# Kernel tuning notes

Hardware: AMD Instinct MI355X
Metric: run time of the kernel (lower is better)

## Reference

```python
import jax, jax.numpy as jnp
import numpy as np

N_PARTICLES = 256
N_DIM = 3
N_KERNELS = 256   # hidden_dim
N_TOUT = 20       # number of time RBF kernels (n_out)
CUTOFF = 5.0
GAMMA = 0.3
BATCH = 4

# off-diagonal column indices: idx[i, j] = j + (j >= i), shape [N, N-1]
_cols = np.arange(N_PARTICLES - 1)
OFFDIAG_IDX = _cols[None, :] + (_cols[None, :] >= np.arange(N_PARTICLES)[:, None])


def setup_inputs() -> dict:
    key = jax.random.key(0)
    k1, k2, k3 = jax.random.split(key, 3)
    x = jax.random.normal(k1, (BATCH, N_PARTICLES * N_DIM), dtype=jnp.float32)
    t = jax.random.uniform(k2, (BATCH,), dtype=jnp.float32)
    weights = jax.random.normal(k3, (N_KERNELS, N_TOUT), dtype=jnp.float32) * np.sqrt(1.0 / N_KERNELS)
    bias = jnp.zeros((1, N_TOUT), dtype=jnp.float32)
    importance = jnp.zeros((N_KERNELS,), dtype=jnp.float32)
    mus = jnp.linspace(0.0, CUTOFF, N_KERNELS, dtype=jnp.float32)
    neg_log_gammas = -jnp.log(GAMMA * jnp.ones((N_KERNELS,), dtype=jnp.float32))
    mus_time = jnp.linspace(0.0, 1.0, N_TOUT, dtype=jnp.float32)
    neg_log_gammas_time = -jnp.log(GAMMA * jnp.ones((N_TOUT,), dtype=jnp.float32))
    return dict(x=x, t=t, weights=weights, bias=bias, importance=importance,
                mus=mus, neg_log_gammas=neg_log_gammas,
                mus_time=mus_time, neg_log_gammas_time=neg_log_gammas_time)


def _rbf_kernels(d, mu, neg_log_gamma):
    # d: [..., 1], mu/neg_log_gamma: [K] -> normalized kernels [..., K]
    inv_gamma2 = jnp.exp(neg_log_gamma) ** 2
    rbfs = jnp.exp(-(d - mu) ** 2 * inv_gamma2)
    return rbfs / (1e-6 + rbfs.sum(axis=-1, keepdims=True))


def reference(x, t, weights, bias, importance, mus, neg_log_gammas,
              mus_time, neg_log_gammas_time):
    B = x.shape[0]
    xp = x.reshape(B, N_PARTICLES, N_DIM)
    # all-pairs distance vectors x_i - x_j, then drop the diagonal -> [B, N, N-1, D]
    r_full = xp[:, :, None, :] - xp[:, None, :, :]
    r = r_full[:, jnp.arange(N_PARTICLES)[:, None], OFFDIAG_IDX, :]
    # distances [B, N, N-1, 1]
    d = jnp.sqrt((r ** 2).sum(axis=-1) + 1e-6)[..., None]
    # normalized distance RBFs [B, N, N-1, K]
    kernels = _rbf_kernels(d, mus, neg_log_gammas)
    # force magnitude over time-output channels [B, N, N-1, T]
    force_mag = (kernels + importance ** 2) @ weights + bias
    # time RBFs [B, T] -> weight and reduce over T
    trbfs = _rbf_kernels(t[:, None], mus_time, neg_log_gammas_time)
    force_mag = (force_mag * trbfs[:, None, None, :]).sum(axis=-1, keepdims=True)
    # weighted aggregation over neighbor axis -> forces [B, N, D]
    forces = (r * force_mag).sum(axis=-2)
    return forces
```

## Files before the change

### kernel.cpp

```cpp
#include <hip/hip_runtime.h>
#include <hip/hip_bf16.h>
#include <stdint.h>

#define NP     256
#define NK     256
#define NT     20
#define BATCHN 4
#define LOG2E  1.44269504088896340736f

typedef __hip_bfloat16 bf16;
typedef float v2f __attribute__((ext_vector_type(2)));

__device__ __forceinline__ bool probe_f32(const void* mus) {
    return ((const uint32_t*)mus)[0] == 0u;
}

__device__ __forceinline__ float ldf(const void* p, int idx, bool f32) {
    return f32 ? ((const float*)p)[idx]
               : __bfloat162float(((const bf16*)p)[idx]);
}

__global__ __launch_bounds__(256)
void vf_fused(const void* __restrict__ x,     const void* __restrict__ t_in,
              const void* __restrict__ weights, const void* __restrict__ bias,
              const void* __restrict__ importance, const void* __restrict__ mus,
              const void* __restrict__ nlg,   const void* __restrict__ mus_t,
              const void* __restrict__ nlg_t, void* __restrict__ out)
{
    const int tid = threadIdx.x;
    const int b   = blockIdx.x >> 8;
    const int i   = blockIdx.x & 255;
    const bool f32 = probe_f32(mus);

    __shared__ __align__(16) float s_pos[NP * 3];
    __shared__ __align__(16) float s_mu[NK];
    __shared__ __align__(16) float s_wp[NK];
    __shared__ float s_traw[NT];
    __shared__ float s_trbf[NT];
    __shared__ float s_redc[4];
    __shared__ float s_redf[12];
    __shared__ float s_constv;

    for (int idx = tid; idx < NP * 3; idx += 256)
        s_pos[idx] = ldf(x, b * NP * 3 + idx, f32);

    if (tid < NT) {
        float tv = ldf(t_in, b, f32);
        float mt = ldf(mus_t, tid, f32);
        float gt = __expf(ldf(nlg_t, tid, f32));
        float dd = tv - mt;
        s_traw[tid] = __expf(-dd * dd * gt * gt);
    }
    __syncthreads();
    if (tid < NT) {
        float s = 0.f;
        #pragma unroll
        for (int tt = 0; tt < NT; ++tt) s += s_traw[tt];
        s_trbf[tid] = s_traw[tid] / (1e-6f + s);
    }
    __syncthreads();

    {
        const int k = tid;
        float wp = 0.f;
        #pragma unroll
        for (int tt = 0; tt < NT; ++tt)
            wp = fmaf(ldf(weights, k * NT + tt, f32), s_trbf[tt], wp);

        s_mu[k] = ldf(mus, k, f32);
        s_wp[k] = wp;

        float imp = ldf(importance, k, f32);
        float v = imp * imp * wp;
        if (k < NT) v = fmaf(s_trbf[k], ldf(bias, k, f32), v);
        #pragma unroll
        for (int off = 32; off > 0; off >>= 1) v += __shfl_down(v, off);
        if ((k & 63) == 0) s_redc[k >> 6] = v;
    }
    __syncthreads();
    if (tid == 0) s_constv = s_redc[0] + s_redc[1] + s_redc[2] + s_redc[3];
    __syncthreads();

    const float g  = __expf(ldf(nlg, 0, f32));
    const float na = -(g * g) * LOG2E;

    float fx = 0.f, fy = 0.f, fz = 0.f;
    if (tid < NP - 1) {
        const int j = tid + (tid >= i ? 1 : 0);
        const float rx = s_pos[i * 3 + 0] - s_pos[j * 3 + 0];
        const float ry = s_pos[i * 3 + 1] - s_pos[j * 3 + 1];
        const float rz = s_pos[i * 3 + 2] - s_pos[j * 3 + 2];
        const float q  = rx * rx + ry * ry + rz * rz + 1e-6f;
        const float d  = sqrtf(q);

        const float4* mu4 = (const float4*)s_mu;
        const float4* wp4 = (const float4*)s_wp;
        const v2f d2v = {d, d};
        const v2f na2 = {na, na};
        v2f normA = {0.f, 0.f}, normB = {0.f, 0.f};
        v2f numA  = {0.f, 0.f}, numB  = {0.f, 0.f};

        #pragma unroll 4
        for (int p = 0; p < NK / 4; ++p) {
            const float4 m = mu4[p];
            const float4 w = wp4[p];
            const v2f muA = {m.x, m.y}, muB = {m.z, m.w};
            const v2f wpA = {w.x, w.y}, wpB = {w.z, w.w};
            const v2f dmA = d2v - muA, dmB = d2v - muB;
            const v2f agA = dmA * dmA * na2;
            const v2f agB = dmB * dmB * na2;
            const v2f eA = {exp2f(agA.x), exp2f(agA.y)};
            const v2f eB = {exp2f(agB.x), exp2f(agB.y)};
            normA += eA; normB += eB;
            numA  += eA * wpA;
            numB  += eB * wpB;
        }
        const float norm = normA.x + normA.y + normB.x + normB.y;
        const float num  = numA.x  + numA.y  + numB.x  + numB.y;
        const float fs = num / (1e-6f + norm) + s_constv;
        fx = rx * fs; fy = ry * fs; fz = rz * fs;
    }

    #pragma unroll
    for (int off = 32; off > 0; off >>= 1) {
        fx += __shfl_down(fx, off);
        fy += __shfl_down(fy, off);
        fz += __shfl_down(fz, off);
    }
    if ((tid & 63) == 0) {
        const int w = tid >> 6;
        s_redf[w * 3 + 0] = fx;
        s_redf[w * 3 + 1] = fy;
        s_redf[w * 3 + 2] = fz;
    }
    __syncthreads();
    if (tid < 3) {
        const float fv = s_redf[tid] + s_redf[3 + tid] + s_redf[6 + tid] + s_redf[9 + tid];
        const int o = (b * NP + i) * 3 + tid;
        if (f32) ((float*)out)[o] = fv;
        else     ((bf16*)out)[o]  = __float2bfloat16(fv);
    }
}

extern "C" void kernel_launch(void* const* d_in, const int* in_sizes, int n_in,
                              void* d_out, int out_size, void* d_ws, size_t ws_size,
                              hipStream_t stream)
{
    vf_fused<<<dim3(BATCHN * NP), dim3(256), 0, stream>>>(
        d_in[0], d_in[1], d_in[2], d_in[3], d_in[4],
        d_in[5], d_in[6], d_in[7], d_in[8], d_out);
}
```

Measured before the change: 93.13 us.

## Split per-batch time-weight precompute into separate prep kernel feeding force kernel

Moves the time-RBF weighting, the per-kernel weight projection and the constant term into a small prep kernel that runs once per batch and writes interleaved mu/wp pairs to workspace. The force kernel then reads those directly from global/L2 instead of recomputing them in every one of 1024 blocks, and drops the shared-memory staging and most syncthreads. It adds a second launch and relies on the workspace being large enough, with a fallback to the old fused kernel otherwise. Inner-loop operands now come from global memory instead of LDS, which may cost latency.

Result: no change. 94.42 us (+1.4%).

```diff
diff --git a/kernel.cpp b/kernel.cpp
--- a/kernel.cpp
+++ b/kernel.cpp
@@ -18,6 +18,132 @@
 __device__ __forceinline__ float ldf(const void* p, int idx, bool f32) {
     return f32 ? ((const float*)p)[idx]
                : __bfloat162float(((const bf16*)p)[idx]);
+}
+
+__global__ __launch_bounds__(256)
+void vf_prep(const void* __restrict__ t_in, const void* __restrict__ weights,
+             const void* __restrict__ bias, const void* __restrict__ importance,
+             const void* __restrict__ mus,  const void* __restrict__ mus_t,
+             const void* __restrict__ nlg_t, float* __restrict__ ws)
+{
+    const int tid = threadIdx.x;
+    const int b   = blockIdx.x;
+    const bool f32 = probe_f32(mus);
+
+    __shared__ float s_traw[NT];
+    __shared__ float s_trbf[NT];
+    __shared__ float s_redc[4];
+
+    if (tid < NT) {
+        float tv = ldf(t_in, b, f32);
+        float mt = ldf(mus_t, tid, f32);
+        float gt = __expf(ldf(nlg_t, tid, f32));
+        float dd = tv - mt;
+        s_traw[tid] = __expf(-dd * dd * gt * gt);
+    }
+    __syncthreads();
+    if (tid < NT) {
+        float s = 0.f;
+        #pragma unroll
+        for (int tt = 0; tt < NT; ++tt) s += s_traw[tt];
+        s_trbf[tid] = s_traw[tid] / (1e-6f + s);
+    }
+    __syncthreads();
+
+    const int k = tid;
+    float wp = 0.f;
+    #pragma unroll
+    for (int tt = 0; tt < NT; ++tt)
+        wp = fmaf(ldf(weights, k * NT + tt, f32), s_trbf[tt], wp);
+
+    float* cw = ws + b * (NK * 2);
+    cw[(k >> 2) * 8 + (k & 3)]     = ldf(mus, k, f32);
+    cw[(k >> 2) * 8 + 4 + (k & 3)] = wp;
+
+    float imp = ldf(importance, k, f32);
+    float v = imp * imp * wp;
+    if (k < NT) v = fmaf(s_trbf[k], ldf(bias, k, f32), v);
+    #pragma unroll
+    for (int off = 32; off > 0; off >>= 1) v += __shfl_down(v, off);
+    if ((k & 63) == 0) s_redc[k >> 6] = v;
+    __syncthreads();
+    if (tid == 0)
+        ws[BATCHN * NK * 2 + b] = s_redc[0] + s_redc[1] + s_redc[2] + s_redc[3];
+}
+
+__global__ __launch_bounds__(256)
+void vf_force(const void* __restrict__ x,  const void* __restrict__ mus,
+              const void* __restrict__ nlg, const float* __restrict__ ws,
+              void* __restrict__ out)
+{
+    const int tid = threadIdx.x;
+    const int b   = blockIdx.x >> 8;
+    const int i   = blockIdx.x & 255;
+    const bool f32 = probe_f32(mus);
+
+    __shared__ float s_redf[12];
+
+    const int xb = b * NP * 3;
+    const float pix = ldf(x, xb + i * 3 + 0, f32);
+    const float piy = ldf(x, xb + i * 3 + 1, f32);
+    const float piz = ldf(x, xb + i * 3 + 2, f32);
+
+    const int j = (tid < NP - 1) ? tid + (tid >= i ? 1 : 0) : i;
+    const float rx = pix - ldf(x, xb + j * 3 + 0, f32);
+    const float ry = piy - ldf(x, xb + j * 3 + 1, f32);
+    const float rz = piz - ldf(x, xb + j * 3 + 2, f32);
+    const float q  = rx * rx + ry * ry + rz * rz + 1e-6f;
+    const float d  = sqrtf(q);
+
+    const float g  = __expf(ldf(nlg, 0, f32));
+    const float na = -(g * g) * LOG2E;
+
+    const float4* cw4 = (const float4*)(ws + b * (NK * 2));
+    const v2f d2v = {d, d};
+    const v2f na2 = {na, na};
+    v2f normA = {0.f, 0.f}, normB = {0.f, 0.f};
+    v2f numA  = {0.f, 0.f}, numB  = {0.f, 0.f};
+
+    #pragma unroll 4
+    for (int p = 0; p < NK / 4; ++p) {
+        const float4 m = cw4[2 * p];
+        const float4 w = cw4[2 * p + 1];
+        const v2f muA = {m.x, m.y}, muB = {m.z, m.w};
+        const v2f wpA = {w.x, w.y}, wpB = {w.z, w.w};
+        const v2f dmA = d2v - muA, dmB = d2v - muB;
+        const v2f agA = dmA * dmA * na2;
+        const v2f agB = dmB * dmB * na2;
+        const v2f eA = {exp2f(agA.x), exp2f(agA.y)};
+        const v2f eB = {exp2f(agB.x), exp2f(agB.y)};
+        normA += eA; normB += eB;
+        numA  += eA * wpA;
+        numB  += eB * wpB;
+    }
+    const float norm = normA.x + normA.y + normB.x + normB.y;
+    const float num  = numA.x  + numA.y  + numB.x  + numB.y;
+    float fs = num / (1e-6f + norm) + ws[BATCHN * NK * 2 + b];
+    if (tid >= NP - 1) fs = 0.f;
+    float fx = rx * fs, fy = ry * fs, fz = rz * fs;
+
+    #pragma unroll
+    for (int off = 32; off > 0; off >>= 1) {
+        fx += __shfl_down(fx, off);
+        fy += __shfl_down(fy, off);
+        fz += __shfl_down(fz, off);
+    }
+    if ((tid & 63) == 0) {
+        const int w = tid >> 6;
+        s_redf[w * 3 + 0] = fx;
+        s_redf[w * 3 + 1] = fy;
+        s_redf[w * 3 + 2] = fz;
+    }
+    __syncthreads();
+    if (tid < 3) {
+        const float fv = s_redf[tid] + s_redf[3 + tid] + s_redf[6 + tid] + s_redf[9 + tid];
+        const int o = (b * NP + i) * 3 + tid;
+        if (f32) ((float*)out)[o] = fv;
+        else     ((bf16*)out)[o]  = __float2bfloat16(fv);
+    }
 }
 
 __global__ __launch_bounds__(256)
@@ -66,10 +192,8 @@
         #pragma unroll
         for (int tt = 0; tt < NT; ++tt)
             wp = fmaf(ldf(weights, k * NT + tt, f32), s_trbf[tt], wp);
-
         s_mu[k] = ldf(mus, k, f32);
         s_wp[k] = wp;
-
         float imp = ldf(importance, k, f32);
         float v = imp * imp * wp;
         if (k < NT) v = fmaf(s_trbf[k], ldf(bias, k, f32), v);
@@ -146,7 +270,16 @@
                               void* d_out, int out_size, void* d_ws, size_t ws_size,
                               hipStream_t stream)
 {
-    vf_fused<<<dim3(BATCHN * NP), dim3(256), 0, stream>>>(
-        d_in[0], d_in[1], d_in[2], d_in[3], d_in[4],
-        d_in[5], d_in[6], d_in[7], d_in[8], d_out);
-}
+    const size_t ws_need = (size_t)(BATCHN * NK * 2 + BATCHN) * sizeof(float);
+    if (d_ws != nullptr && ws_size >= ws_need) {
+        float* ws = (float*)d_ws;
+        vf_prep<<<dim3(BATCHN), dim3(256), 0, stream>>>(
+            d_in[1], d_in[2], d_in[3], d_in[4], d_in[5], d_in[7], d_in[8], ws);
+        vf_force<<<dim3(BATCHN * NP), dim3(256), 0, stream>>>(
+            d_in[0], d_in[5], d_in[6], ws, d_out);
+    } else {
+        vf_fused<<<dim3(BATCHN * NP), dim3(256), 0, stream>>>(
+            d_in[0], d_in[1], d_in[2], d_in[3], d_in[4],
+            d_in[5], d_in[6], d_in[7], d_in[8], d_out);
+    }
+}
```
